# Performance work log

Hardware: AMD Instinct MI355X
Metric: run time of the kernel (lower is better)

## Reference

```python
import jax, jax.numpy as jnp
from jax import lax
import numpy as np

DEPTH = 4
D_MODEL = 192
D_INNER = 384
D_STATE = 16
D_CONV = 4
DT_RANK = 12
STRIDE = 4
NUM_PATCHES = 400
L_SEQ = NUM_PATCHES + 1  # +1 cls token appended at the end
EPS = 1e-5


def _rmsnorm(x, w):
    x = x.astype(jnp.float32)
    return (x * lax.rsqrt(jnp.mean(x * x, axis=-1, keepdims=True) + EPS)) * w


def _mamba(x, in_w, cw, cb, xp_w, dtw, dtb, A_log, Dv, ow):
    # x: [B, L, D_MODEL]
    B = x.shape[0]
    xz = jnp.einsum('bld,ed->ble', x, in_w)            # [B, L, 2*D_INNER]
    u, z = jnp.split(xz, 2, axis=-1)                   # [B, L, D_INNER] each
    # causal depthwise conv over L
    u_t = jnp.transpose(u, (0, 2, 1))                  # [B, D_INNER, L]
    u_pad = jnp.pad(u_t, ((0, 0), (0, 0), (D_CONV - 1, 0)))
    conv = lax.conv_general_dilated(
        u_pad, cw[:, None, :], (1,), 'VALID',
        dimension_numbers=('NCH', 'OIH', 'NCH'),
        feature_group_count=D_INNER)                   # [B, D_INNER, L]
    u = jax.nn.silu(conv + cb[:, None])
    u = jnp.transpose(u, (0, 2, 1))                    # [B, L, D_INNER]
    xdbl = jnp.einsum('bld,ed->ble', u, xp_w)          # [B, L, 44]
    dt, Bm, Cm = jnp.split(xdbl, [DT_RANK, DT_RANK + D_STATE], axis=-1)
    dt = jax.nn.softplus(jnp.einsum('blr,dr->bld', dt, dtw) + dtb)  # [B, L, D_INNER]
    A = -jnp.exp(A_log)                                # [D_INNER, D_STATE]
    dA = jnp.exp(dt[..., None] * A)                    # [B, L, D_INNER, D_STATE]
    dBu = dt[..., None] * Bm[:, :, None, :] * u[..., None]
    h0 = jnp.zeros((B, D_INNER, D_STATE), dtype=dA.dtype)

    def step(h, inp):
        dA_t, dBu_t = inp
        h = dA_t * h + dBu_t
        return h, h

    _, hs = lax.scan(step, h0, (jnp.swapaxes(dA, 0, 1), jnp.swapaxes(dBu, 0, 1)))
    hs = jnp.swapaxes(hs, 0, 1)                        # [B, L, D_INNER, D_STATE]
    y = jnp.einsum('bldn,bln->bld', hs, Cm) + u * Dv
    y = y * jax.nn.silu(z)
    return jnp.einsum('bld,ed->ble', y, ow)            # [B, L, D_MODEL]


def _forward(imgs, patch_w, patch_b, pos_embed, cls_token, norm_w, in_proj_w,
             conv_w, conv_b, xproj_w, dt_w, dt_b, A_log, D_param, out_w,
             normf_w, head_w, head_b):
    B = imgs.shape[0]
    # StrideEmbed: non-overlapping strides of 4 bytes -> linear to embed_dim
    x = imgs.reshape(B, NUM_PATCHES, STRIDE) @ patch_w + patch_b  # [B, 400, 192]
    x = x + pos_embed[:, :-1, :]
    cls = cls_token + pos_embed[:, -1:, :]             # [1, 1, 192]
    x = jnp.concatenate([x, jnp.broadcast_to(cls, (B, 1, D_MODEL))], axis=1)
    hidden = x
    residual = None
    for i in range(DEPTH):
        residual = hidden if residual is None else hidden + residual  # fp32 residual stream
        h = _rmsnorm(residual, norm_w[i])
        hidden = _mamba(h, in_proj_w[i], conv_w[i], conv_b[i], xproj_w[i],
                        dt_w[i], dt_b[i], A_log[i], D_param[i], out_w[i])
    x = _rmsnorm(hidden + residual, normf_w)
    cls_out = x[:, -1, :]                              # [B, 192]
    logits = cls_out @ head_w.T + head_b               # [B, 1000]
    return logits


def setup_inputs() -> dict:
    key = jax.random.key(0)
    ks = jax.random.split(key, 16)
    B = 32
    rn = lambda k, s, sc: jax.random.normal(k, s, dtype=jnp.float32) * sc
    A_log = jnp.broadcast_to(jnp.log(jnp.arange(1.0, D_STATE + 1.0, dtype=jnp.float32)),
                             (DEPTH, D_INNER, D_STATE))
    return {
        'imgs': rn(ks[0], (B, 1, 40, 40), 1.0),
        'patch_w': rn(ks[1], (STRIDE, D_MODEL), 0.1),
        'patch_b': jnp.zeros((D_MODEL,), jnp.float32),
        'pos_embed': rn(ks[2], (1, L_SEQ, D_MODEL), 0.02),
        'cls_token': rn(ks[3], (1, 1, D_MODEL), 0.02),
        'norm_w': jnp.ones((DEPTH, D_MODEL), jnp.float32),
        'in_proj_w': rn(ks[4], (DEPTH, 2 * D_INNER, D_MODEL), 0.05),
        'conv_w': rn(ks[5], (DEPTH, D_INNER, D_CONV), 0.3),
        'conv_b': jnp.zeros((DEPTH, D_INNER), jnp.float32),
        'xproj_w': rn(ks[6], (DEPTH, DT_RANK + 2 * D_STATE, D_INNER), 0.05),
        'dt_w': rn(ks[7], (DEPTH, D_INNER, DT_RANK), 0.1),
        'dt_b': rn(ks[8], (DEPTH, D_INNER), 0.5) - 4.0,
        'A_log': A_log,
        'D_param': jnp.ones((DEPTH, D_INNER), jnp.float32),
        'out_w': rn(ks[9], (DEPTH, D_MODEL, D_INNER), 0.05),
        'normf_w': jnp.ones((D_MODEL,), jnp.float32),
        'head_w': rn(ks[10], (1000, D_MODEL), 0.05),
        'head_b': jnp.zeros((1000,), jnp.float32),
    }


def reference(imgs, patch_w, patch_b, pos_embed, cls_token, norm_w, in_proj_w,
              conv_w, conv_b, xproj_w, dt_w, dt_b, A_log, D_param, out_w,
              normf_w, head_w, head_b):
    return _forward(imgs, patch_w, patch_b, pos_embed, cls_token, norm_w,
                    in_proj_w, conv_w, conv_b, xproj_w, dt_w, dt_b, A_log,
                    D_param, out_w, normf_w, head_w, head_b)
```

## Files before the change

### kernel.cpp

```cpp
#include <hip/hip_runtime.h>
#include <hip/hip_bf16.h>

#define B_SZ 32
#define LSEQ 401
#define NT (B_SZ * LSEQ)
#define DM 192
#define DI 384
#define DS 16
#define EPSF 1e-5f
#define NCH 16
#define TCMAX 26

typedef __attribute__((ext_vector_type(8))) short short8;
typedef __attribute__((ext_vector_type(4))) float f32x4;
typedef __hip_bfloat16 bf16;

#define OFF_IMGS    0
#define OFF_PATCHW  51200
#define OFF_PATCHB  51968
#define OFF_POS     52160
#define OFF_CLS     129152
#define OFF_NORMW   129344
#define OFF_INW     130112
#define OFF_CONVW   719936
#define OFF_CONVB   726080
#define OFF_XPROJW  727616
#define OFF_DTW     795200
#define OFF_DTB     813632
#define OFF_ALOG    815168
#define OFF_DP      839744
#define OFF_OUTW    841280
#define OFF_NORMF   1136192
#define OFF_HEADW   1136384
#define OFF_HEADB   1328384
#define OFF_TOTAL   1329384

#define WB_INW   0
#define WB_XPJ   589824
#define WB_OUT   688128
#define WB_DTW   983040
#define WB_TOTAL 1032192

__device__ __forceinline__ int chunk_s(int c) { return c == 0 ? 0 : 25 * c + 1; }
__device__ __forceinline__ int chunk_e(int c) { return 25 * c + 26; }

__device__ __forceinline__ float ldsrc(const void* p, int off, int isbf) {
  return isbf ? __bfloat162float(((const bf16*)p)[off]) : ((const float*)p)[off];
}
__device__ __forceinline__ float fast_silu(float z) {
  return z * __builtin_amdgcn_rcpf(1.f + __expf(-z));
}
__device__ __forceinline__ float fast_softplus(float x) {
  float e = __expf(x);
  return (x > 15.f) ? x : __logf(1.f + e);
}
__device__ __forceinline__ float bfbits(unsigned short u) {
  return __uint_as_float(((unsigned int)u) << 16);
}

#define DPP_ADD(x, ctrl) \
  x += __int_as_float(__builtin_amdgcn_update_dpp(0, __float_as_int(x), ctrl, 0xF, 0xF, true))
__device__ __forceinline__ float row_sum16(float x) {
  DPP_ADD(x, 0xB1);
  DPP_ADD(x, 0x4E);
  DPP_ADD(x, 0x124);
  DPP_ADD(x, 0x128);
  return x;
}

struct P18 { const void* p[18]; };

__global__ __launch_bounds__(256) void k_convwb(P18 t, float* __restrict__ fin,
                                                bf16* __restrict__ wb) {
  static const int st[19] = {OFF_IMGS, OFF_PATCHW, OFF_PATCHB, OFF_POS, OFF_CLS,
                             OFF_NORMW, OFF_INW, OFF_CONVW, OFF_CONVB, OFF_XPROJW,
                             OFF_DTW, OFF_DTB, OFF_ALOG, OFF_DP, OFF_OUTW,
                             OFF_NORMF, OFF_HEADW, OFF_HEADB, OFF_TOTAL};
  int isbf = (((const unsigned short*)t.p[5])[0] == 0x3F80) ? 1 : 0;
  int idx = blockIdx.x * 256 + threadIdx.x;
  if (idx < OFF_TOTAL) {
    int lo = 0;
#pragma unroll
    for (int i = 1; i < 18; ++i) if (idx >= st[i]) lo = i;
    fin[idx] = ldsrc(t.p[lo], idx - st[lo], isbf);
  } else if (idx < OFF_TOTAL + WB_TOTAL) {
    int j = idx - OFF_TOTAL;
    float v;
    if (j < WB_XPJ) {
      v = ldsrc(t.p[6], j, isbf);
    } else if (j < WB_OUT) {
      int i2 = j - WB_XPJ;
      int l = i2 / (64 * 384);
      int r = (i2 / 384) & 63;
      int k = i2 % 384;
      v = (r < 44) ? ldsrc(t.p[9], l * 44 * 384 + r * 384 + k, isbf) : 0.f;
    } else if (j < WB_DTW) {
      v = ldsrc(t.p[14], j - WB_OUT, isbf);
    } else {
      int i2 = j - WB_DTW;
      int l = i2 / (384 * 32);
      int r = i2 % (384 * 32);
      int d = r >> 5;
      int k = r & 31;
      v = (k < 12) ? ldsrc(t.p[10], l * 4608 + d * 12 + k, isbf) : 0.f;
    }
    wb[j] = __float2bfloat16(v);
  }
}

__device__ __forceinline__ void inproj_4w(const bf16 (*shb)[200],
                                          const bf16* __restrict__ Win,
                                          bf16* __restrict__ xb,
                                          bf16* __restrict__ zb,
                                          int row0, int tid) {
  int lane = tid & 63, wave = tid >> 6;
  int q = lane >> 4, mlo = lane & 15;
  short8 afrA[6], afrB[6];
#pragma unroll
  for (int kk = 0; kk < 6; ++kk) {
    afrA[kk] = *(const short8*)&shb[mlo][kk * 32 + q * 8];
    afrB[kk] = *(const short8*)&shb[16 + mlo][kk * 32 + q * 8];
  }
  const bf16* wbase = Win + (size_t)(wave * 192 + mlo) * DM + q * 8;
  bf16* dst = (wave < 2) ? xb : zb;
  int ncol0 = (wave < 2) ? wave * 192 : (wave - 2) * 192;
#pragma unroll
  for (int jh = 0; jh < 4; ++jh) {
    short8 Bb[18];
#pragma unroll
    for (int j = 0; j < 3; ++j)
#pragma unroll
      for (int kk = 0; kk < 6; ++kk)
        Bb[j * 6 + kk] = *(const short8*)(wbase + (size_t)(jh * 3 + j) * 16 * DM + kk * 32);
#pragma unroll
    for (int j = 0; j < 3; ++j) {
      f32x4 aA = {}, aB = {};
#pragma unroll
      for (int kk = 0; kk < 6; ++kk) {
        aA = __builtin_amdgcn_mfma_f32_16x16x32_bf16(afrA[kk], Bb[j * 6 + kk], aA, 0, 0, 0);
        aB = __builtin_amdgcn_mfma_f32_16x16x32_bf16(afrB[kk], Bb[j * 6 + kk], aB, 0, 0, 0);
      }
      int n = ncol0 + (jh * 3 + j) * 16 + mlo;
#pragma unroll
      for (int i = 0; i < 4; ++i) {
        dst[(size_t)(row0 + q * 4 + i) * DI + n] = __float2bfloat16(aA[i]);
        dst[(size_t)(row0 + 16 + q * 4 + i) * DI + n] = __float2bfloat16(aB[i]);
      }
    }
  }
}

__global__ __launch_bounds__(256)
__attribute__((amdgpu_waves_per_eu(2, 2)))
void k_embedin(const float* __restrict__ fin,
               float* __restrict__ residual,
               const bf16* __restrict__ Win,
               bf16* __restrict__ xb,
               bf16* __restrict__ zb) {
  __shared__ bf16 shb[32][200];
  const float* imgs = fin + OFF_IMGS;
  const float* pw   = fin + OFF_PATCHW;
  const float* pb   = fin + OFF_PATCHB;
  const float* pos  = fin + OFF_POS;
  const float* cls  = fin + OFF_CLS;
  const float* nw0  = fin + OFF_NORMW;
  int tid = threadIdx.x;
  int row0 = blockIdx.x * 32;
#pragma unroll
  for (int rr = 0; rr < 2; ++rr) {
    int row = rr * 16 + (tid >> 4), g = tid & 15;
    int t = row0 + row;
    int b = t / LSEQ, l = t % LSEQ;
    float im[4];
    if (l < 400) {
#pragma unroll
      for (int s = 0; s < 4; ++s) im[s] = imgs[b * 1600 + l * 4 + s];
    }
    float rn[12], ss = 0.f;
#pragma unroll
    for (int k = 0; k < 12; ++k) {
      int col = g + 16 * k;
      float v;
      if (l < 400) {
        v = pb[col] + pos[l * DM + col];
#pragma unroll
        for (int s = 0; s < 4; ++s) v = fmaf(im[s], pw[s * DM + col], v);
      } else {
        v = cls[col] + pos[400 * DM + col];
      }
      residual[(size_t)t * DM + col] = v;
      rn[k] = v;
      ss = fmaf(v, v, ss);
    }
    ss = row_sum16(ss);
    float sres = rsqrtf(ss / (float)DM + EPSF);
#pragma unroll
    for (int k = 0; k < 12; ++k) {
      int col = g + 16 * k;
      shb[row][col] = __float2bfloat16(rn[k] * sres * nw0[col]);
    }
  }
  __syncthreads();
  inproj_4w(shb, Win, xb, zb, row0, tid);
}

__global__ __launch_bounds__(512) void k_xdtA(const bf16* __restrict__ xb,
                                              const float* __restrict__ cw,
                                              const float* __restrict__ cb,
                                              const bf16* __restrict__ Wbf,
                                              float* __restrict__ xdbl,
                                              const bf16* __restrict__ dtwb,
                                              const float* __restrict__ dtb,
                                              const float* __restrict__ A_log,
                                              bf16* __restrict__ ub,
                                              bf16* __restrict__ dto,
                                              float* __restrict__ Pq,
                                              float* __restrict__ Hq) {
  __shared__ __align__(16) bf16  su[32][392];
  __shared__ __align__(16) char  smemB[22752];
  __shared__ __align__(16) float4 scw4[384];
  __shared__ float scb[384];
  __shared__ __align__(16) float sxp[2][32][48];
  __shared__ __align__(16) bf16  sxb[32][32];
  bf16 (*sxt)[392]  = (bf16(*)[392])smemB;
  bf16 (*sdtl)[384] = (bf16(*)[384])smemB;
  float (*sB)[16]   = (float(*)[16])(smemB + 19968);

  int cc = blockIdx.x, b = blockIdx.y;
  int tid = threadIdx.x;
  int s = chunk_s(cc), tc = chunk_e(cc) - s;
  int base = b * LSEQ;

  for (int i = tid; i < (tc + 3) * 48; i += 512) {
    int r = i / 48, c8 = i - r * 48;
    int tt = s - 3 + r;
    if (tt < 0) tt = 0;
    *(short8*)&sxt[r][c8 * 8] = *(const short8*)(xb + (size_t)(base + tt) * DI + c8 * 8);
  }
  {
    short8 z = {};
    for (int i = tid; i < (32 - tc) * 48; i += 512) {
      int r = tc + i / 48, c8 = i % 48;
      *(short8*)&su[r][c8 * 8] = z;
    }
  }
  for (int i = tid; i < 384; i += 512) {
    scw4[i] = ((const float4*)cw)[i];
    scb[i] = cb[i];
  }
  __syncthreads();
  for (int i = tid; i < tc * 48; i += 512) {
    int tok = i / 48, c8 = i % 48, d0 = c8 * 8;
    int l = s + tok;
    float xr[4][8];
#pragma unroll
    for (int k = 0; k < 4; ++k) {
      short8 v = *(const short8*)&sxt[tok + k][d0];
      bool ok = (l - 3 + k) >= 0;
#pragma unroll
      for (int j = 0; j < 8; ++j) {
        unsigned int uu = ((unsigned int)(unsigned short)v[j]) << 16;
        xr[k][j] = ok ? __uint_as_float(uu) : 0.f;
      }
    }
    short8 uvv;
#pragma unroll
    for (int j = 0; j < 8; ++j) {
      float4 w = scw4[d0 + j];
      float a = scb[d0 + j];
      a = fmaf(xr[0][j], w.x, a);
      a = fmaf(xr[1][j], w.y, a);
      a = fmaf(xr[2][j], w.z, a);
      a = fmaf(xr[3][j], w.w, a);
      bf16 h = __float2bfloat16(fast_silu(a));
      uvv[j] = *reinterpret_cast<short*>(&h);
    }
    *(short8*)&su[tok][d0] = uvv;
    *(short8*)(ub + (size_t)(base + l) * DI + d0) = uvv;
  }
  __syncthreads();
  int lane = tid & 63, wave = tid >> 6;
  int q = lane >> 4, mlo = lane & 15;
  for (int j = wave; j < 12; j += 8) {
    int rt = j / 6, rem = j % 6, kh = rem / 3, cg = rem % 3;
    f32x4 acc = {};
    for (int k0 = 0; k0 < 192; k0 += 32) {
      short8 a = *(const short8*)&su[rt * 16 + mlo][kh * 192 + k0 + q * 8];
      short8 bb = *(const short8*)(Wbf + (size_t)(cg * 16 + mlo) * DI + kh * 192 + k0 + q * 8);
      acc = __builtin_amdgcn_mfma_f32_16x16x32_bf16(a, bb, acc, 0, 0, 0);
    }
#pragma unroll
    for (int i = 0; i < 4; ++i) sxp[kh][rt * 16 + q * 4 + i][cg * 16 + mlo] = acc[i];
  }
  __syncthreads();
  for (int i = tid; i < tc * 44; i += 512) {
    int r = i / 44, c = i % 44;
    xdbl[(size_t)(base + s + r) * 44 + c] = sxp[0][r][c] + sxp[1][r][c];
  }
  for (int i = tid; i < tc * 16; i += 512) {
    int t = i >> 4, col = i & 15;
    sB[t][col] = sxp[0][t][12 + col] + sxp[1][t][12 + col];
  }
  for (int i = tid; i < 1024; i += 512) {
    int tok = i >> 5, k = i & 31;
    sxb[tok][k] = __float2bfloat16((k < 12 && tok < tc) ? sxp[0][tok][k] + sxp[1][tok][k] : 0.f);
  }
  __syncthreads();
#pragma unroll
  for (int jt = 0; jt < 6; ++jt) {
    int job = wave + jt * 8;
    int rt = job / 24, nt = job % 24;
    int d = nt * 16 + mlo;
    short8 afrag = *(const short8*)&sxb[rt * 16 + mlo][q * 8];
    short8 bfrag = *(const short8*)(dtwb + (size_t)d * 32 + q * 8);
    f32x4 acc = {};
    acc = __builtin_amdgcn_mfma_f32_16x16x32_bf16(afrag, bfrag, acc, 0, 0, 0);
    float dtbv = dtb[d];
#pragma unroll
    for (int i = 0; i < 4; ++i) {
      int row = rt * 16 + q * 4 + i;
      if (row < tc) {
        bf16 hv = __float2bfloat16(fast_softplus(acc[i] + dtbv));
        dto[(size_t)(base + s + row) * DI + d] = hv;
        sdtl[row][d] = hv;
      }
    }
  }
  __syncthreads();
  if (cc < NCH - 1 && tid < 384) {
    int d = tid;
    float A[16], h[16];
#pragma unroll
    for (int j = 0; j < 4; ++j) {
      f32x4 al = *(const f32x4*)&A_log[d * DS + j * 4];
#pragma unroll
      for (int i = 0; i < 4; ++i) { A[j * 4 + i] = -__expf(al[i]); h[j * 4 + i] = 0.f; }
    }
    float S = 0.f;
    for (int t = 0; t < tc; ++t) {
      float dv = bfbits(*(const unsigned short*)&sdtl[t][d]);
      float uv = bfbits(*(const unsigned short*)&su[t][d]);
      float w = dv * uv;
      S += dv;
      f32x4 B0 = *(const f32x4*)&sB[t][0];
      f32x4 B1 = *(const f32x4*)&sB[t][4];
      f32x4 B2 = *(const f32x4*)&sB[t][8];
      f32x4 B3 = *(const f32x4*)&sB[t][12];
#pragma unroll
      for (int n = 0; n < 16; ++n) {
        float Bn = (n < 4) ? B0[n] : (n < 8) ? B1[n - 4] : (n < 12) ? B2[n - 8] : B3[n - 12];
        float E = __expf(dv * A[n]);
        h[n] = fmaf(E, h[n], w * Bn);
      }
    }
    size_t si = (((size_t)cc * B_SZ + b) * 384 + d) * 16;
#pragma unroll
    for (int j = 0; j < 4; ++j) {
      f32x4 hv, pv;
#pragma unroll
      for (int i = 0; i < 4; ++i) {
        hv[i] = h[j * 4 + i];
        pv[i] = __expf(A[j * 4 + i] * S);
      }
      *(f32x4*)&Hq[si + j * 4] = hv;
      *(f32x4*)&Pq[si + j * 4] = pv;
    }
  }
}

__global__ __launch_bounds__(256) void k_scanP(const float* __restrict__ Pq,
                                               float* __restrict__ Hq) {
  int idx = blockIdx.x * 256 + threadIdx.x;
  int n = idx & 15;
  int dd = (idx >> 4) % 384;
  int b = idx / (384 * 16);
  float hs = 0.f;
  for (int c = 0; c < NCH - 1; ++c) {
    size_t hi = ((((size_t)c * B_SZ + b) * 384 + dd) * 16) + n;
    float P = Pq[hi];
    float he = Hq[hi];
    hs = fmaf(P, hs, he);
    Hq[hi] = hs;
  }
}

__global__ __launch_bounds__(384)
void k_scanB(const bf16* __restrict__ zb,
             const bf16* __restrict__ ub,
             const bf16* __restrict__ dtv,
             const float* __restrict__ xdbl,
             const float* __restrict__ A_log,
             const float* __restrict__ Dp,
             const float* __restrict__ Hq,
             bf16* __restrict__ yb) {
  __shared__ bf16 sdt[TCMAX][384], su[TCMAX][384], sz[TCMAX][384];
  __shared__ float sB[TCMAX][16], sC[TCMAX][16];
  int cc = blockIdx.x, b = blockIdx.y;
  int d = threadIdx.x;
  int s = chunk_s(cc), tc = chunk_e(cc) - s;
  int base = b * LSEQ;
  int ng = tc * 48;
#pragma unroll
  for (int j = 0; j < 4; ++j) {
    int i = d + j * 384;
    if (i < ng) {
      int r = i / 48, c8 = i - r * 48;
      size_t g = (size_t)(base + s + r) * DI + c8 * 8;
      *(short8*)&sdt[r][c8 * 8] = *(const short8*)(dtv + g);
      *(short8*)&su[r][c8 * 8]  = *(const short8*)(ub + g);
      *(short8*)&sz[r][c8 * 8]  = *(const short8*)(zb + g);
    }
  }
  for (int i = d; i < tc * 32; i += 384) {
    int t = i >> 5, col = i & 31;
    float v = xdbl[(size_t)(base + s + t) * 44 + 12 + col];
    if (col < 16) sB[t][col] = v;
    else          sC[t][col - 16] = v;
  }
  __syncthreads();
  float A[16], h[16];
#pragma unroll
  for (int j = 0; j < 4; ++j) {
    f32x4 al = *(const f32x4*)&A_log[d * DS + j * 4];
#pragma unroll
    for (int i = 0; i < 4; ++i) { A[j * 4 + i] = -__expf(al[i]); h[j * 4 + i] = 0.f; }
  }
  if (cc > 0) {
    size_t hi = (((size_t)(cc - 1) * B_SZ + b) * 384 + d) * 16;
#pragma unroll
    for (int j = 0; j < 4; ++j) {
      f32x4 hv = *(const f32x4*)&Hq[hi + j * 4];
#pragma unroll
      for (int i = 0; i < 4; ++i) h[j * 4 + i] = hv[i];
    }
  }
  float Dv = Dp[d];
  bf16* py = yb + (size_t)(base + s) * DI + d;
  for (int t = 0; t < tc; ++t) {
    float dv = bfbits(*(const unsigned short*)&sdt[t][d]);
    float uv = bfbits(*(const unsigned short*)&su[t][d]);
    float zv = bfbits(*(const unsigned short*)&sz[t][d]);
    float w = dv * uv;
    f32x4 B0 = *(const f32x4*)&sB[t][0];
    f32x4 B1 = *(const f32x4*)&sB[t][4];
    f32x4 B2 = *(const f32x4*)&sB[t][8];
    f32x4 B3 = *(const f32x4*)&sB[t][12];
    f32x4 C0 = *(const f32x4*)&sC[t][0];
    f32x4 C1 = *(const f32x4*)&sC[t][4];
    f32x4 C2 = *(const f32x4*)&sC[t][8];
    f32x4 C3 = *(const f32x4*)&sC[t][12];
    float y0 = 0.f, y1 = 0.f;
#pragma unroll
    for (int n = 0; n < 16; ++n) {
      float Bn = (n < 4) ? B0[n] : (n < 8) ? B1[n - 4] : (n < 12) ? B2[n - 8] : B3[n - 12];
      float Cn = (n < 4) ? C0[n] : (n < 8) ? C1[n - 4] : (n < 12) ? C2[n - 8] : C3[n - 12];
      float E = __expf(dv * A[n]);
      h[n] = fmaf(E, h[n], w * Bn);
      if (n & 1) y1 = fmaf(h[n], Cn, y1);
      else       y0 = fmaf(h[n], Cn, y0);
    }
    float yv = (y0 + y1 + uv * Dv) * fast_silu(zv);
    py[(size_t)t * DI] = __float2bfloat16(yv);
  }
}

__global__ __launch_bounds__(256)
__attribute__((amdgpu_waves_per_eu(2, 2)))
void k_outin(const bf16* __restrict__ yb,
             const bf16* __restrict__ Wout,
             float* __restrict__ residual,
             const float* __restrict__ nw,
             const bf16* __restrict__ Win,
             bf16* __restrict__ xb,
             bf16* __restrict__ zb) {
  __shared__ bf16  syt[32][392];
  __shared__ float sCt[32][200];
  __shared__ bf16  shb[32][200];
  int tid = threadIdx.x;
  int lane = tid & 63;
  int wave = tid >> 6;
  int row0 = blockIdx.x * 32;
  int q = lane >> 4;
  int mlo = lane & 15;
  {
    const bf16* src = yb + (size_t)row0 * DI;
    short8 v[6];
#pragma unroll
    for (int j = 0; j < 6; ++j) {
      int i = tid + j * 256;
      v[j] = *(const short8*)(src + (i / 48) * DI + (i % 48) * 8);
    }
#pragma unroll
    for (int j = 0; j < 6; ++j) {
      int i = tid + j * 256;
      *(short8*)&syt[i / 48][(i % 48) * 8] = v[j];
    }
  }
  __syncthreads();
  {
    int colw = wave * 48;
    f32x4 acc[2][3] = {};
#pragma unroll
    for (int kh = 0; kh < 2; ++kh) {
      const bf16* brow = Wout + (size_t)(colw + mlo) * DI + kh * 192 + q * 8;
      short8 Bf[18];
#pragma unroll
      for (int j = 0; j < 3; ++j)
#pragma unroll
        for (int k2 = 0; k2 < 6; ++k2)
          Bf[j * 6 + k2] = *(const short8*)(brow + (size_t)j * 16 * DI + k2 * 32);
      short8 afA[6], afB[6];
#pragma unroll
      for (int k2 = 0; k2 < 6; ++k2) {
        afA[k2] = *(const short8*)&syt[mlo][kh * 192 + k2 * 32 + q * 8];
        afB[k2] = *(const short8*)&syt[16 + mlo][kh * 192 + k2 * 32 + q * 8];
      }
#pragma unroll
      for (int k2 = 0; k2 < 6; ++k2) {
#pragma unroll
        for (int j = 0; j < 3; ++j) {
          acc[0][j] = __builtin_amdgcn_mfma_f32_16x16x32_bf16(afA[k2], Bf[j * 6 + k2], acc[0][j], 0, 0, 0);
          acc[1][j] = __builtin_amdgcn_mfma_f32_16x16x32_bf16(afB[k2], Bf[j * 6 + k2], acc[1][j], 0, 0, 0);
        }
      }
    }
#pragma unroll
    for (int rg = 0; rg < 2; ++rg)
#pragma unroll
      for (int j = 0; j < 3; ++j)
#pragma unroll
        for (int i = 0; i < 4; ++i)
          sCt[rg * 16 + q * 4 + i][colw + j * 16 + mlo] = acc[rg][j][i];
  }
  __syncthreads();
#pragma unroll
  for (int rr = 0; rr < 2; ++rr) {
    int row = rr * 16 + (tid >> 4), g = tid & 15;
    int t = row0 + row;
    float* rp = residual + (size_t)t * DM + g * 12;
    float4 r4[3];
#pragma unroll
    for (int j = 0; j < 3; ++j) r4[j] = *(const float4*)(rp + j * 4);
    float rn[12], ss = 0.f;
#pragma unroll
    for (int k = 0; k < 12; ++k) {
      int col = g * 12 + k;
      float x = sCt[row][col] + ((const float*)r4)[k];
      rn[k] = x;
      ss = fmaf(x, x, ss);
    }
    ss = row_sum16(ss);
    float sres = rsqrtf(ss / (float)DM + EPSF);
#pragma unroll
    for (int j = 0; j < 3; ++j) {
      float4 w4;
      w4.x = rn[j * 4 + 0]; w4.y = rn[j * 4 + 1];
      w4.z = rn[j * 4 + 2]; w4.w = rn[j * 4 + 3];
      *(float4*)(rp + j * 4) = w4;
    }
#pragma unroll
    for (int k = 0; k < 12; ++k) {
      int col = g * 12 + k;
      shb[row][col] = __float2bfloat16(rn[k] * sres * nw[col]);
    }
  }
  __syncthreads();
  inproj_4w(shb, Win, xb, zb, row0, tid);
}

__global__ __launch_bounds__(256) void k_lastout(const bf16* __restrict__ yb,
                                                 const bf16* __restrict__ Wout,
                                                 const float* __restrict__ resIn,
                                                 float* __restrict__ clsbuf) {
  __shared__ float sCt[16][200];
  int tid = threadIdx.x;
  int lane = tid & 63;
  int wave = tid >> 6;
  int b0 = blockIdx.x * 16;
  int q = lane >> 4;
  int mlo = lane & 15;
  int colw = wave * 48;
  f32x4 acc[3] = {};
  const bf16* arow = yb + ((size_t)(b0 + mlo) * LSEQ + 400) * DI + q * 8;
  for (int k0 = 0; k0 < DI; k0 += 32) {
    short8 a = *(const short8*)(arow + k0);
#pragma unroll
    for (int j = 0; j < 3; ++j) {
      short8 b = *(const short8*)(Wout + (size_t)(colw + j * 16 + mlo) * DI + k0 + q * 8);
      acc[j] = __builtin_amdgcn_mfma_f32_16x16x32_bf16(a, b, acc[j], 0, 0, 0);
    }
  }
#pragma unroll
  for (int j = 0; j < 3; ++j)
#pragma unroll
    for (int i = 0; i < 4; ++i) sCt[q * 4 + i][colw + j * 16 + mlo] = acc[j][i];
  __syncthreads();
  int row = tid >> 4, g = tid & 15;
  int bb = b0 + row;
#pragma unroll
  for (int k = 0; k < 12; ++k) {
    int col = g + 16 * k;
    clsbuf[(size_t)bb * DM + col] =
        sCt[row][col] + resIn[((size_t)bb * LSEQ + 400) * DM + col];
  }
}

__global__ __launch_bounds__(256) void k_final(const float* __restrict__ clsbuf,
                                               const float* __restrict__ fin,
                                               const void* __restrict__ nw_raw,
                                               void* __restrict__ out) {
  const float* normf  = fin + OFF_NORMF;
  const float* head_w = fin + OFF_HEADW;
  const float* head_b = fin + OFF_HEADB;
  __shared__ float clsv[DM];
  __shared__ float partial[4];
  __shared__ float sres;
  int b = blockIdx.x;
  float r = 0.f;
  if (threadIdx.x < DM) r = clsbuf[(size_t)b * DM + threadIdx.x];
  float ss = r * r;
#pragma unroll
  for (int m = 32; m >= 1; m >>= 1) ss += __shfl_xor(ss, m, 64);
  if ((threadIdx.x & 63) == 0) partial[threadIdx.x >> 6] = ss;
  __syncthreads();
  if (threadIdx.x == 0)
    sres = rsqrtf((partial[0] + partial[1] + partial[2] + partial[3]) / (float)DM + EPSF);
  __syncthreads();
  if (threadIdx.x < DM) clsv[threadIdx.x] = r * sres * normf[threadIdx.x];
  __syncthreads();
  int isbf = (((const unsigned short*)nw_raw)[0] == 0x3F80) ? 1 : 0;
  for (int e = threadIdx.x; e < 1000; e += 256) {
    float acc = head_b[e];
    for (int k = 0; k < DM; ++k) acc = fmaf(clsv[k], head_w[e * DM + k], acc);
    if (isbf) ((bf16*)out)[b * 1000 + e] = __float2bfloat16(acc);
    else      ((float*)out)[b * 1000 + e] = acc;
  }
}

extern "C" void kernel_launch(void* const* d_in, const int* in_sizes, int n_in,
                              void* d_out, int out_size, void* d_ws, size_t ws_size,
                              hipStream_t stream) {
  char* base = (char*)d_ws;
  size_t off = 0;
  auto alloc = [&](size_t bytes) { char* p = base + off; off = (off + bytes + 255) & ~(size_t)255; return p; };
  float* fin      = (float*)alloc((size_t)OFF_TOTAL * 4);
  bf16*  wb       = (bf16*)alloc((size_t)WB_TOTAL * 2);
  float* residual = (float*)alloc((size_t)NT * DM * 4);
  bf16*  xb       = (bf16*)alloc((size_t)NT * DI * 2);
  bf16*  zb       = (bf16*)alloc((size_t)NT * DI * 2);
  bf16*  ub       = (bf16*)alloc((size_t)NT * DI * 2);
  float* xdbl     = (float*)alloc((size_t)NT * 44 * 4);
  bf16*  dtb16    = (bf16*)alloc((size_t)NT * DI * 2);
  float* Pq       = (float*)alloc((size_t)(NCH - 1) * B_SZ * 384 * 16 * 4);
  float* Hq       = (float*)alloc((size_t)(NCH - 1) * B_SZ * 384 * 16 * 4);
  float* clsbuf   = (float*)alloc((size_t)B_SZ * DM * 4);
  bf16*  yb       = ub;

  P18 t;
  for (int i = 0; i < 18; ++i) t.p[i] = d_in[i];
  k_convwb<<<(OFF_TOTAL + WB_TOTAL + 255) / 256, 256, 0, stream>>>(t, fin, wb);

  k_embedin<<<NT / 32, 256, 0, stream>>>(fin, residual, wb + WB_INW, xb, zb);

  for (int layer = 0; layer < 4; ++layer) {
    const float* dtb = fin + OFF_DTB + layer * DI;
    const float* alog = fin + OFF_ALOG + layer * DI * DS;

    k_xdtA<<<dim3(NCH, B_SZ), 512, 0, stream>>>(xb, fin + OFF_CONVW + layer * DI * 4,
                                                fin + OFF_CONVB + layer * DI,
                                                wb + WB_XPJ + layer * 64 * DI, xdbl,
                                                wb + WB_DTW + layer * 384 * 32, dtb,
                                                alog, ub, dtb16, Pq, Hq);

    k_scanP<<<(B_SZ * 384 * 16) / 256, 256, 0, stream>>>(Pq, Hq);
    k_scanB<<<dim3(NCH, B_SZ), 384, 0, stream>>>(zb, ub, dtb16, xdbl, alog,
                                                 fin + OFF_DP + layer * DI, Hq, yb);

    if (layer < 3) {
      k_outin<<<NT / 32, 256, 0, stream>>>(yb, wb + WB_OUT + layer * DM * DI, residual,
                                           fin + OFF_NORMW + (layer + 1) * DM,
                                           wb + WB_INW + (layer + 1) * 768 * DM, xb, zb);
    } else {
      k_lastout<<<2, 256, 0, stream>>>(yb, wb + WB_OUT + 3 * DM * DI, residual, clsbuf);
    }
  }
  k_final<<<B_SZ, 256, 0, stream>>>(clsbuf, fin, d_in[5], d_out);
}
```

Before: 533.2 us.

## Fuse chunked selective scan with out-proj, residual RMSNorm and in-proj

```diff
diff --git a/kernel.cpp b/kernel.cpp
--- a/kernel.cpp
+++ b/kernel.cpp
@@ -384,6 +384,205 @@
   }
 }
 
+__global__ __launch_bounds__(384) void k_scanOI(const bf16* __restrict__ zb_in,
+                                                const bf16* __restrict__ ub,
+                                                const bf16* __restrict__ dtv,
+                                                const float* __restrict__ xdbl,
+                                                const float* __restrict__ A_log,
+                                                const float* __restrict__ Dp,
+                                                const float* __restrict__ Hq,
+                                                const bf16* __restrict__ Wout,
+                                                float* __restrict__ residual,
+                                                const float* __restrict__ nw,
+                                                const bf16* __restrict__ Win,
+                                                bf16* __restrict__ xb,
+                                                bf16* __restrict__ zb_out) {
+  __shared__ __align__(16) char smem[67840];
+  bf16  (*sdt)[384] = (bf16(*)[384])smem;
+  float (*sCt)[192] = (float(*)[192])smem;
+  bf16  (*suy)[384] = (bf16(*)[384])(smem + 19968);
+  bf16  (*szs)[384] = (bf16(*)[384])(smem + 44544);
+  bf16  (*shb)[200] = (bf16(*)[200])(smem + 44544);
+  float (*sB)[16]   = (float(*)[16])(smem + 64512);
+  float (*sC)[16]   = (float(*)[16])(smem + 66176);
+
+  int cc = blockIdx.x, b = blockIdx.y;
+  int tid = threadIdx.x;
+  int lane = tid & 63, wave = tid >> 6;
+  int q = lane >> 4, mlo = lane & 15;
+  int s = chunk_s(cc), tc = chunk_e(cc) - s;
+  int base = b * LSEQ;
+
+  int ng = tc * 48;
+#pragma unroll
+  for (int j = 0; j < 4; ++j) {
+    int i = tid + j * 384;
+    if (i < ng) {
+      int r = i / 48, c8 = i - r * 48;
+      size_t g = (size_t)(base + s + r) * DI + c8 * 8;
+      *(short8*)&sdt[r][c8 * 8] = *(const short8*)(dtv + g);
+      *(short8*)&suy[r][c8 * 8] = *(const short8*)(ub + g);
+      *(short8*)&szs[r][c8 * 8] = *(const short8*)(zb_in + g);
+    }
+  }
+  {
+    short8 z = {};
+    for (int i = tid; i < (32 - tc) * 48; i += 384) {
+      int r = tc + i / 48, c8 = i % 48;
+      *(short8*)&suy[r][c8 * 8] = z;
+    }
+  }
+  for (int i = tid; i < tc * 32; i += 384) {
+    int t = i >> 5, col = i & 31;
+    float v = xdbl[(size_t)(base + s + t) * 44 + 12 + col];
+    if (col < 16) sB[t][col] = v;
+    else          sC[t][col - 16] = v;
+  }
+  __syncthreads();
+  {
+    int d = tid;
+    float A[16], h[16];
+#pragma unroll
+    for (int j = 0; j < 4; ++j) {
+      f32x4 al = *(const f32x4*)&A_log[d * DS + j * 4];
+#pragma unroll
+      for (int i = 0; i < 4; ++i) { A[j * 4 + i] = -__expf(al[i]); h[j * 4 + i] = 0.f; }
+    }
+    if (cc > 0) {
+      size_t hi = (((size_t)(cc - 1) * B_SZ + b) * 384 + d) * 16;
+#pragma unroll
+      for (int j = 0; j < 4; ++j) {
+        f32x4 hv = *(const f32x4*)&Hq[hi + j * 4];
+#pragma unroll
+        for (int i = 0; i < 4; ++i) h[j * 4 + i] = hv[i];
+      }
+    }
+    float Dv = Dp[d];
+    for (int t = 0; t < tc; ++t) {
+      float dv = bfbits(*(const unsigned short*)&sdt[t][d]);
+      float uv = bfbits(*(const unsigned short*)&suy[t][d]);
+      float zv = bfbits(*(const unsigned short*)&szs[t][d]);
+      float w = dv * uv;
+      f32x4 B0 = *(const f32x4*)&sB[t][0];
+      f32x4 B1 = *(const f32x4*)&sB[t][4];
+      f32x4 B2 = *(const f32x4*)&sB[t][8];
+      f32x4 B3 = *(const f32x4*)&sB[t][12];
+      f32x4 C0 = *(const f32x4*)&sC[t][0];
+      f32x4 C1 = *(const f32x4*)&sC[t][4];
+      f32x4 C2 = *(const f32x4*)&sC[t][8];
+      f32x4 C3 = *(const f32x4*)&sC[t][12];
+      float y0 = 0.f, y1 = 0.f;
+#pragma unroll
+      for (int n = 0; n < 16; ++n) {
+        float Bn = (n < 4) ? B0[n] : (n < 8) ? B1[n - 4] : (n < 12) ? B2[n - 8] : B3[n - 12];
+        float Cn = (n < 4) ? C0[n] : (n < 8) ? C1[n - 4] : (n < 12) ? C2[n - 8] : C3[n - 12];
+        float E = __expf(dv * A[n]);
+        h[n] = fmaf(E, h[n], w * Bn);
+        if (n & 1) y1 = fmaf(h[n], Cn, y1);
+        else       y0 = fmaf(h[n], Cn, y0);
+      }
+      float yv = (y0 + y1 + uv * Dv) * fast_silu(zv);
+      bf16 yh = __float2bfloat16(yv);
+      suy[t][d] = yh;
+    }
+  }
+  __syncthreads();
+#pragma unroll
+  for (int jt = 0; jt < 4; ++jt) {
+    int job = wave + jt * 6;
+    int ct = job % 12, rg = job / 12;
+    int colw = ct * 16;
+    const bf16* brow = Wout + (size_t)(colw + mlo) * DI + q * 8;
+    short8 Bf[12];
+#pragma unroll
+    for (int k2 = 0; k2 < 12; ++k2) Bf[k2] = *(const short8*)(brow + k2 * 32);
+    f32x4 acc = {};
+#pragma unroll
+    for (int k2 = 0; k2 < 12; ++k2) {
+      short8 a = *(const short8*)&suy[rg * 16 + mlo][k2 * 32 + q * 8];
+      acc = __builtin_amdgcn_mfma_f32_16x16x32_bf16(a, Bf[k2], acc, 0, 0, 0);
+    }
+#pragma unroll
+    for (int i = 0; i < 4; ++i) {
+      int row = rg * 16 + q * 4 + i;
+      if (row < tc) sCt[row][colw + mlo] = acc[i];
+    }
+  }
+  __syncthreads();
+  {
+    int g = tid & 15;
+    for (int r = tid >> 4; r < tc; r += 24) {
+      int t = base + s + r;
+      float* rp = residual + (size_t)t * DM + g * 12;
+      float4 r4[3];
+#pragma unroll
+      for (int j = 0; j < 3; ++j) r4[j] = *(const float4*)(rp + j * 4);
+      float rn[12], ss = 0.f;
+#pragma unroll
+      for (int k = 0; k < 12; ++k) {
+        float x = sCt[r][g * 12 + k] + ((const float*)r4)[k];
+        rn[k] = x;
+        ss = fmaf(x, x, ss);
+      }
+      ss = row_sum16(ss);
+      float sres = rsqrtf(ss / (float)DM + EPSF);
+#pragma unroll
+      for (int j = 0; j < 3; ++j) {
+        float4 w4;
+        w4.x = rn[j * 4 + 0]; w4.y = rn[j * 4 + 1];
+        w4.z = rn[j * 4 + 2]; w4.w = rn[j * 4 + 3];
+        *(float4*)(rp + j * 4) = w4;
+      }
+#pragma unroll
+      for (int k = 0; k < 12; ++k) {
+        int col = g * 12 + k;
+        shb[r][col] = __float2bfloat16(rn[k] * sres * nw[col]);
+      }
+    }
+    for (int i = tid; i < (32 - tc) * 200; i += 384) {
+      shb[tc + i / 200][i % 200] = __float2bfloat16(0.f);
+    }
+  }
+  __syncthreads();
+  {
+    short8 afrA[6], afrB[6];
+#pragma unroll
+    for (int kk = 0; kk < 6; ++kk) {
+      afrA[kk] = *(const short8*)&shb[mlo][kk * 32 + q * 8];
+      afrB[kk] = *(const short8*)&shb[16 + mlo][kk * 32 + q * 8];
+    }
+    const bf16* wbase = Win + (size_t)(wave * 128 + mlo) * DM + q * 8;
+    bf16* dst = (wave < 3) ? xb : zb_out;
+    int ncol0 = (wave < 3) ? wave * 128 : (wave - 3) * 128;
+#pragma unroll
+    for (int jh = 0; jh < 4; ++jh) {
+      short8 Bb[12];
+#pragma unroll
+      for (int j = 0; j < 2; ++j)
+#pragma unroll
+        for (int kk = 0; kk < 6; ++kk)
+          Bb[j * 6 + kk] = *(const short8*)(wbase + (size_t)(jh * 2 + j) * 16 * DM + kk * 32);
+#pragma unroll
+      for (int j = 0; j < 2; ++j) {
+        f32x4 aA = {}, aB = {};
+#pragma unroll
+        for (int kk = 0; kk < 6; ++kk) {
+          aA = __builtin_amdgcn_mfma_f32_16x16x32_bf16(afrA[kk], Bb[j * 6 + kk], aA, 0, 0, 0);
+          aB = __builtin_amdgcn_mfma_f32_16x16x32_bf16(afrB[kk], Bb[j * 6 + kk], aB, 0, 0, 0);
+        }
+        int n = ncol0 + (jh * 2 + j) * 16 + mlo;
+#pragma unroll
+        for (int i = 0; i < 4; ++i) {
+          int rA = q * 4 + i;
+          int rB = 16 + q * 4 + i;
+          if (rA < tc) dst[(size_t)(base + s + rA) * DI + n] = __float2bfloat16(aA[i]);
+          if (rB < tc) dst[(size_t)(base + s + rB) * DI + n] = __float2bfloat16(aB[i]);
+        }
+      }
+    }
+  }
+}
+
 __global__ __launch_bounds__(384)
 void k_scanB(const bf16* __restrict__ zb,
              const bf16* __restrict__ ub,
@@ -462,110 +661,6 @@
     float yv = (y0 + y1 + uv * Dv) * fast_silu(zv);
     py[(size_t)t * DI] = __float2bfloat16(yv);
   }
-}
-
-__global__ __launch_bounds__(256)
-__attribute__((amdgpu_waves_per_eu(2, 2)))
-void k_outin(const bf16* __restrict__ yb,
-             const bf16* __restrict__ Wout,
-             float* __restrict__ residual,
-             const float* __restrict__ nw,
-             const bf16* __restrict__ Win,
-             bf16* __restrict__ xb,
-             bf16* __restrict__ zb) {
-  __shared__ bf16  syt[32][392];
-  __shared__ float sCt[32][200];
-  __shared__ bf16  shb[32][200];
-  int tid = threadIdx.x;
-  int lane = tid & 63;
-  int wave = tid >> 6;
-  int row0 = blockIdx.x * 32;
-  int q = lane >> 4;
-  int mlo = lane & 15;
-  {
-    const bf16* src = yb + (size_t)row0 * DI;
-    short8 v[6];
-#pragma unroll
-    for (int j = 0; j < 6; ++j) {
-      int i = tid + j * 256;
-      v[j] = *(const short8*)(src + (i / 48) * DI + (i % 48) * 8);
-    }
-#pragma unroll
-    for (int j = 0; j < 6; ++j) {
-      int i = tid + j * 256;
-      *(short8*)&syt[i / 48][(i % 48) * 8] = v[j];
-    }
-  }
-  __syncthreads();
-  {
-    int colw = wave * 48;
-    f32x4 acc[2][3] = {};
-#pragma unroll
-    for (int kh = 0; kh < 2; ++kh) {
-      const bf16* brow = Wout + (size_t)(colw + mlo) * DI + kh * 192 + q * 8;
-      short8 Bf[18];
-#pragma unroll
-      for (int j = 0; j < 3; ++j)
-#pragma unroll
-        for (int k2 = 0; k2 < 6; ++k2)
-          Bf[j * 6 + k2] = *(const short8*)(brow + (size_t)j * 16 * DI + k2 * 32);
-      short8 afA[6], afB[6];
-#pragma unroll
-      for (int k2 = 0; k2 < 6; ++k2) {
-        afA[k2] = *(const short8*)&syt[mlo][kh * 192 + k2 * 32 + q * 8];
-        afB[k2] = *(const short8*)&syt[16 + mlo][kh * 192 + k2 * 32 + q * 8];
-      }
-#pragma unroll
-      for (int k2 = 0; k2 < 6; ++k2) {
-#pragma unroll
-        for (int j = 0; j < 3; ++j) {
-          acc[0][j] = __builtin_amdgcn_mfma_f32_16x16x32_bf16(afA[k2], Bf[j * 6 + k2], acc[0][j], 0, 0, 0);
-          acc[1][j] = __builtin_amdgcn_mfma_f32_16x16x32_bf16(afB[k2], Bf[j * 6 + k2], acc[1][j], 0, 0, 0);
-        }
-      }
-    }
-#pragma unroll
-    for (int rg = 0; rg < 2; ++rg)
-#pragma unroll
-      for (int j = 0; j < 3; ++j)
-#pragma unroll
-        for (int i = 0; i < 4; ++i)
-          sCt[rg * 16 + q * 4 + i][colw + j * 16 + mlo] = acc[rg][j][i];
-  }
-  __syncthreads();
-#pragma unroll
-  for (int rr = 0; rr < 2; ++rr) {
-    int row = rr * 16 + (tid >> 4), g = tid & 15;
-    int t = row0 + row;
-    float* rp = residual + (size_t)t * DM + g * 12;
-    float4 r4[3];
-#pragma unroll
-    for (int j = 0; j < 3; ++j) r4[j] = *(const float4*)(rp + j * 4);
-    float rn[12], ss = 0.f;
-#pragma unroll
-    for (int k = 0; k < 12; ++k) {
-      int col = g * 12 + k;
-      float x = sCt[row][col] + ((const float*)r4)[k];
-      rn[k] = x;
-      ss = fmaf(x, x, ss);
-    }
-    ss = row_sum16(ss);
-    float sres = rsqrtf(ss / (float)DM + EPSF);
-#pragma unroll
-    for (int j = 0; j < 3; ++j) {
-      float4 w4;
-      w4.x = rn[j * 4 + 0]; w4.y = rn[j * 4 + 1];
-      w4.z = rn[j * 4 + 2]; w4.w = rn[j * 4 + 3];
-      *(float4*)(rp + j * 4) = w4;
-    }
-#pragma unroll
-    for (int k = 0; k < 12; ++k) {
-      int col = g * 12 + k;
-      shb[row][col] = __float2bfloat16(rn[k] * sres * nw[col]);
-    }
-  }
-  __syncthreads();
-  inproj_4w(shb, Win, xb, zb, row0, tid);
 }
 
 __global__ __launch_bounds__(256) void k_lastout(const bf16* __restrict__ yb,
@@ -665,6 +760,7 @@
   for (int layer = 0; layer < 4; ++layer) {
     const float* dtb = fin + OFF_DTB + layer * DI;
     const float* alog = fin + OFF_ALOG + layer * DI * DS;
+    const float* dp = fin + OFF_DP + layer * DI;
 
     k_xdtA<<<dim3(NCH, B_SZ), 512, 0, stream>>>(xb, fin + OFF_CONVW + layer * DI * 4,
                                                 fin + OFF_CONVB + layer * DI,
@@ -673,14 +769,15 @@
                                                 alog, ub, dtb16, Pq, Hq);
 
     k_scanP<<<(B_SZ * 384 * 16) / 256, 256, 0, stream>>>(Pq, Hq);
-    k_scanB<<<dim3(NCH, B_SZ), 384, 0, stream>>>(zb, ub, dtb16, xdbl, alog,
-                                                 fin + OFF_DP + layer * DI, Hq, yb);
 
     if (layer < 3) {
-      k_outin<<<NT / 32, 256, 0, stream>>>(yb, wb + WB_OUT + layer * DM * DI, residual,
-                                           fin + OFF_NORMW + (layer + 1) * DM,
-                                           wb + WB_INW + (layer + 1) * 768 * DM, xb, zb);
+      k_scanOI<<<dim3(NCH, B_SZ), 384, 0, stream>>>(zb, ub, dtb16, xdbl, alog, dp, Hq,
+                                                    wb + WB_OUT + layer * DM * DI, residual,
+                                                    fin + OFF_NORMW + (layer + 1) * DM,
+                                                    wb + WB_INW + (layer + 1) * 768 * DM,
+                                                    xb, zb);
     } else {
+      k_scanB<<<dim3(NCH, B_SZ), 384, 0, stream>>>(zb, ub, dtb16, xdbl, alog, dp, Hq, yb);
       k_lastout<<<2, 256, 0, stream>>>(yb, wb + WB_OUT + 3 * DM * DI, residual, clsbuf);
     }
   }
```

After: 562.7 us. 5.5% more time.
